# Kernel tuning notes

Measured on AMD Instinct MI355X. Metric: run time of the kernel, lower is better.

## Reference

```python
import jax, jax.numpy as jnp
import numpy as np

T = 1.0  # temperature (default in original forward)


def setup_inputs() -> dict:
    key = jax.random.key(0)
    k1, k2 = jax.random.split(key)
    N, M, D = 65536, 512, 256
    z = jax.random.normal(k1, (N, D), dtype=jnp.float32)
    e = jax.random.normal(k2, (M, D), dtype=jnp.float32)
    log_sigma = jnp.zeros((1,), dtype=jnp.float32)  # init_log_sigma = 0.0
    return {"z": z, "e": e, "log_sigma": log_sigma}


def reference(z, e, log_sigma):
    N, z_dim = z.shape
    M = e.shape[0]
    # pad N up to a multiple of M (zeros), then view as [B, M, z_dim]
    N_pad = ((N + M - 1) // M) * M
    z = jnp.pad(z, ((0, N_pad - N), (0, 0)))
    zb = z.reshape(-1, M, z_dim)  # [B, M, D]
    # squared euclidean distance via GEMM form: ||z||^2 + ||e||^2 - 2 z.e -> [B, M, M]
    dist = (
        jnp.sum(zb * zb, axis=-1)[:, :, None]
        + jnp.sum(e * e, axis=-1)[None, None, :]
        - 2.0 * jnp.einsum("bmd,kd->bmk", zb, e)
    )
    alpha = -1.0 / (2.0 * jnp.exp(log_sigma[0]) ** 2)
    # logsumexp over the z-block dim (axis=1), mean over codebook dim (axis=1 after reduce)
    loss = -jnp.mean(T * jax.nn.logsumexp(alpha * dist / T, axis=1), axis=1)  # [B]
    loss = loss + 0.5 * z_dim * (2.0 * log_sigma[0] - 1.0) + jnp.log(jnp.float32(M))
    return jnp.mean(loss)
```

## Files before the change

kernel.cpp:

```cpp
#include <hip/hip_runtime.h>
#include <stdint.h>
#include <math.h>

typedef __attribute__((ext_vector_type(8))) short short8;
typedef __attribute__((ext_vector_type(16))) float f32x16;

#define DEVI static __device__ __forceinline__

constexpr int D = 256;

constexpr size_t WS_EIMG  = 0;
constexpr size_t WS_ETERM = 262144;
constexpr size_t WS_WMAX  = 264192;
constexpr size_t WS_WSUM  = WS_WMAX + 1048576;
constexpr size_t WS_PART  = WS_WSUM + 1048576;

DEVI unsigned int f2bf(float f) {
  unsigned int u = __float_as_uint(f);
  return (u + 0x7fffu + ((u >> 16) & 1u)) >> 16;
}
DEVI float shflx(float v, int m) { return __shfl_xor(v, m, 64); }

__global__ void prep_e(const float* __restrict__ e, const float* __restrict__ lsp,
                       char* __restrict__ eimg, float* __restrict__ eterm) {
  const int et = blockIdx.x, t = threadIdx.x;
  const int c = t >> 3, o = t & 7;
  const int gc = et * 32 + c;
  const float a = __expf(-2.0f * lsp[0]);
  const float* s = e + (size_t)gc * D + o * 32;
  float sq = 0.0f;
  unsigned int w[16];
#pragma unroll
  for (int i = 0; i < 8; ++i) {
    float4 x = *(const float4*)(s + i * 4);
    sq += x.x * x.x + x.y * x.y + x.z * x.z + x.w * x.w;
    w[2 * i]     = f2bf(a * x.x) | (f2bf(a * x.y) << 16);
    w[2 * i + 1] = f2bf(a * x.z) | (f2bf(a * x.w) << 16);
  }
  sq += shflx(sq, 1); sq += shflx(sq, 2); sq += shflx(sq, 4);
  char* base = eimg + (size_t)et * 16384;
#pragma unroll
  for (int g = 0; g < 4; ++g) {
    int k2 = o * 4 + g;
    int phys = (c * 512 + k2 * 16) ^ ((c & 7) << 4);
    uint4 pk; pk.x = w[4 * g]; pk.y = w[4 * g + 1];
    pk.z = w[4 * g + 2]; pk.w = w[4 * g + 3];
    *(uint4*)(base + phys) = pk;
  }
  if (o == 0) eterm[gc] = -0.5f * a * sq;
}

__global__ __launch_bounds__(256, 2)
void lse_main(const float* __restrict__ z, const char* __restrict__ eimg,
              const float* __restrict__ lsp, float* __restrict__ wmax,
              float* __restrict__ wsum) {
  __shared__ char  ebuf[2][16384];
  __shared__ float zterm[128];
  __shared__ float pmaxb[2][4][32];
  __shared__ float psumb[2][4][32];

  const int tid = threadIdx.x;
  const int wid = tid >> 6, lane = tid & 63;
  const int l31 = lane & 31;
  const int hi  = lane >> 5;
  const int bx = blockIdx.x;
  const float a = __expf(-2.0f * lsp[0]);

  uint4 er[4];
#pragma unroll
  for (int i = 0; i < 4; ++i)
    er[i] = *(const uint4*)(eimg + i * 4096 + tid * 16);

  short8 A[16];
  const float* zs = z + ((size_t)bx * 128 + wid * 32 + l31) * D + hi * 8;
  float sq = 0.0f;
#pragma unroll
  for (int g = 0; g < 8; ++g) {
#pragma unroll
    for (int s2 = 0; s2 < 2; ++s2) {
      const int s = g * 2 + s2;
      float4 x0 = *(const float4*)(zs + s * 16);
      float4 x1 = *(const float4*)(zs + s * 16 + 4);
      sq += x0.x * x0.x + x0.y * x0.y + x0.z * x0.z + x0.w * x0.w +
            x1.x * x1.x + x1.y * x1.y + x1.z * x1.z + x1.w * x1.w;
      uint4 pk;
      pk.x = f2bf(x0.x) | (f2bf(x0.y) << 16);
      pk.y = f2bf(x0.z) | (f2bf(x0.w) << 16);
      pk.z = f2bf(x1.x) | (f2bf(x1.y) << 16);
      pk.w = f2bf(x1.z) | (f2bf(x1.w) << 16);
      A[s] = __builtin_bit_cast(short8, pk);
    }
    asm volatile("" ::: "memory");
  }
  sq += shflx(sq, 32);
  if (hi == 0) zterm[wid * 32 + l31] = -0.5f * a * sq;

#pragma unroll
  for (int i = 0; i < 4; ++i)
    *(uint4*)(&ebuf[0][0] + i * 4096 + tid * 16) = er[i];
  __syncthreads();

  float zt[16];
#pragma unroll
  for (int r = 0; r < 16; ++r)
    zt[r] = zterm[wid * 32 + (r & 3) + 8 * (r >> 2) + 4 * hi];

  const int cbase = l31 * 512;
  const int key = (l31 & 7) << 4;

  for (int p = 0; p < 16; ++p) {
    const int cur = p & 1;
    if (p < 15) {
#pragma unroll
      for (int i = 0; i < 4; ++i)
        er[i] = *(const uint4*)(eimg + (size_t)(p + 1) * 16384 + i * 4096 + tid * 16);
    }

    f32x16 acc;
#pragma unroll
    for (int i = 0; i < 16; ++i) acc[i] = 0.0f;
    const char* bp = &ebuf[cur][0];
#pragma unroll
    for (int s = 0; s < 16; ++s) {
      short8 B = *(const short8*)(bp + cbase + (((2 * s + hi) * 16) ^ key));
      acc = __builtin_amdgcn_mfma_f32_32x32x16_bf16(A[s], B, acc, 0, 0, 0);
    }

    float mx = -1e30f;
#pragma unroll
    for (int r = 0; r < 16; ++r) {
      acc[r] += zt[r];
      mx = fmaxf(mx, acc[r]);
    }
    mx = fmaxf(mx, shflx(mx, 32));
    float sme = 0.0f;
#pragma unroll
    for (int r = 0; r < 16; ++r) sme += __expf(acc[r] - mx);
    sme += shflx(sme, 32);
    if (hi == 0) {
      pmaxb[cur][wid][l31] = mx;
      psumb[cur][wid][l31] = sme;
    }
    if (p < 15) {
#pragma unroll
      for (int i = 0; i < 4; ++i)
        *(uint4*)(&ebuf[cur ^ 1][0] + i * 4096 + tid * 16) = er[i];
    }
    __syncthreads();

    if (tid < 32) {
      float m0 = pmaxb[cur][0][tid], m1 = pmaxb[cur][1][tid];
      float m2 = pmaxb[cur][2][tid], m3 = pmaxb[cur][3][tid];
      float nm = fmaxf(fmaxf(m0, m1), fmaxf(m2, m3));
      float s = psumb[cur][0][tid] * __expf(m0 - nm) +
                psumb[cur][1][tid] * __expf(m1 - nm) +
                psumb[cur][2][tid] * __expf(m2 - nm) +
                psumb[cur][3][tid] * __expf(m3 - nm);
      wmax[(size_t)bx * 512 + p * 32 + tid] = nm;
      wsum[(size_t)bx * 512 + p * 32 + tid] = s;
    }
  }
}

__global__ void merge_b(const float* __restrict__ wmax, const float* __restrict__ wsum,
                        const float* __restrict__ eterm, float* __restrict__ partial) {
  __shared__ float sh[512];
  const int b = blockIdx.x, t = threadIdx.x;
  float m[4];
  float nm = -1e30f;
#pragma unroll
  for (int i = 0; i < 4; ++i) {
    m[i] = wmax[(size_t)(4 * b + i) * 512 + t];
    nm = fmaxf(nm, m[i]);
  }
  float s = 0.0f;
#pragma unroll
  for (int i = 0; i < 4; ++i)
    s += wsum[(size_t)(4 * b + i) * 512 + t] * __expf(m[i] - nm);
  sh[t] = nm + logf(s) + eterm[t];
  __syncthreads();
  for (int st = 256; st > 0; st >>= 1) {
    if (t < st) sh[t] += sh[t + st];
    __syncthreads();
  }
  if (t == 0) partial[b] = sh[0];
}

__global__ void final_k(const float* __restrict__ partial,
                        const float* __restrict__ lsp, float* __restrict__ out) {
  __shared__ float sh[128];
  const int t = threadIdx.x;
  sh[t] = partial[t];
  __syncthreads();
  for (int st = 64; st > 0; st >>= 1) {
    if (t < st) sh[t] += sh[t + st];
    __syncthreads();
  }
  if (t == 0) {
    float ls = lsp[0];
    out[0] = -sh[0] / 65536.0f + 128.0f * (2.0f * ls - 1.0f) + logf(512.0f);
  }
}

extern "C" void kernel_launch(void* const* d_in, const int* in_sizes, int n_in,
                              void* d_out, int out_size, void* d_ws, size_t ws_size,
                              hipStream_t stream) {
  const float* z   = (const float*)d_in[0];
  const float* e   = (const float*)d_in[1];
  const float* lsp = (const float*)d_in[2];
  float* out = (float*)d_out;
  char* ws = (char*)d_ws;
  char*  eimg    = ws + WS_EIMG;
  float* eterm   = (float*)(ws + WS_ETERM);
  float* wmax    = (float*)(ws + WS_WMAX);
  float* wsum    = (float*)(ws + WS_WSUM);
  float* partial = (float*)(ws + WS_PART);

  prep_e<<<dim3(16), dim3(256), 0, stream>>>(e, lsp, eimg, eterm);
  lse_main<<<dim3(512), dim3(256), 0, stream>>>(z, eimg, lsp, wmax, wsum);
  merge_b<<<dim3(128), dim3(512), 0, stream>>>(wmax, wsum, eterm, partial);
  final_k<<<dim3(1), dim3(128), 0, stream>>>(partial, lsp, out);
}
```

Baseline: 45.49 us.

## Read codebook B-fragments directly from global memory, drop LDS staging and per-tile barriers

The prep kernel now writes the bf16 codebook in MFMA fragment order so each lane can load its B operand straight from global (L2-resident) memory. The main kernel no longer stages codebook tiles through double-buffered LDS and no longer synchronises after every 32-column tile. It processes two tiles per iteration with two independent MFMA accumulators and does one cross-wave merge at the end. This removes LDS traffic and 16 barriers per block, at the cost of more global/L2 load latency inside the MFMA loop and higher register pressure.

```diff
diff --git a/kernel.cpp b/kernel.cpp
--- a/kernel.cpp
+++ b/kernel.cpp
@@ -40,11 +40,11 @@
   sq += shflx(sq, 1); sq += shflx(sq, 2); sq += shflx(sq, 4);
   char* base = eimg + (size_t)et * 16384;
 #pragma unroll
-  for (int g = 0; g < 4; ++g) {
-    int k2 = o * 4 + g;
-    int phys = (c * 512 + k2 * 16) ^ ((c & 7) << 4);
-    uint4 pk; pk.x = w[4 * g]; pk.y = w[4 * g + 1];
-    pk.z = w[4 * g + 2]; pk.w = w[4 * g + 3];
+  for (int i = 0; i < 4; ++i) {
+    int g = o * 4 + i;
+    int phys = (g >> 1) * 1024 + (g & 1) * 512 + c * 16;
+    uint4 pk; pk.x = w[4 * i]; pk.y = w[4 * i + 1];
+    pk.z = w[4 * i + 2]; pk.w = w[4 * i + 3];
     *(uint4*)(base + phys) = pk;
   }
   if (o == 0) eterm[gc] = -0.5f * a * sq;
@@ -54,10 +54,8 @@
 void lse_main(const float* __restrict__ z, const char* __restrict__ eimg,
               const float* __restrict__ lsp, float* __restrict__ wmax,
               float* __restrict__ wsum) {
-  __shared__ char  ebuf[2][16384];
-  __shared__ float zterm[128];
-  __shared__ float pmaxb[2][4][32];
-  __shared__ float psumb[2][4][32];
+  __shared__ float sh_m[4][512];
+  __shared__ float sh_s[4][512];
 
   const int tid = threadIdx.x;
   const int wid = tid >> 6, lane = tid & 63;
@@ -65,11 +63,6 @@
   const int hi  = lane >> 5;
   const int bx = blockIdx.x;
   const float a = __expf(-2.0f * lsp[0]);
-
-  uint4 er[4];
-#pragma unroll
-  for (int i = 0; i < 4; ++i)
-    er[i] = *(const uint4*)(eimg + i * 4096 + tid * 16);
 
   short8 A[16];
   const float* zs = z + ((size_t)bx * 128 + wid * 32 + l31) * D + hi * 8;
@@ -93,72 +86,61 @@
     asm volatile("" ::: "memory");
   }
   sq += shflx(sq, 32);
-  if (hi == 0) zterm[wid * 32 + l31] = -0.5f * a * sq;
-
-#pragma unroll
-  for (int i = 0; i < 4; ++i)
-    *(uint4*)(&ebuf[0][0] + i * 4096 + tid * 16) = er[i];
+  const float term = -0.5f * a * sq;
+
+  float zt[16];
+#pragma unroll
+  for (int r = 0; r < 16; ++r)
+    zt[r] = __shfl(term, (r & 3) + 8 * (r >> 2) + 4 * hi, 64);
+
+  for (int p = 0; p < 8; ++p) {
+    const char* t0 = eimg + (size_t)(2 * p) * 16384 + lane * 16;
+    const char* t1 = t0 + 16384;
+
+    f32x16 acc0, acc1;
+#pragma unroll
+    for (int i = 0; i < 16; ++i) { acc0[i] = 0.0f; acc1[i] = 0.0f; }
+#pragma unroll
+    for (int s = 0; s < 16; ++s) {
+      short8 B0 = *(const short8*)(t0 + s * 1024);
+      short8 B1 = *(const short8*)(t1 + s * 1024);
+      acc0 = __builtin_amdgcn_mfma_f32_32x32x16_bf16(A[s], B0, acc0, 0, 0, 0);
+      acc1 = __builtin_amdgcn_mfma_f32_32x32x16_bf16(A[s], B1, acc1, 0, 0, 0);
+    }
+
+    float mx0 = -1e30f, mx1 = -1e30f;
+#pragma unroll
+    for (int r = 0; r < 16; ++r) {
+      acc0[r] += zt[r]; acc1[r] += zt[r];
+      mx0 = fmaxf(mx0, acc0[r]); mx1 = fmaxf(mx1, acc1[r]);
+    }
+    mx0 = fmaxf(mx0, shflx(mx0, 32));
+    mx1 = fmaxf(mx1, shflx(mx1, 32));
+    float sm0 = 0.0f, sm1 = 0.0f;
+#pragma unroll
+    for (int r = 0; r < 16; ++r) {
+      sm0 += __expf(acc0[r] - mx0);
+      sm1 += __expf(acc1[r] - mx1);
+    }
+    sm0 += shflx(sm0, 32);
+    sm1 += shflx(sm1, 32);
+    if (hi == 0) {
+      sh_m[wid][p * 64 + l31] = mx0;      sh_s[wid][p * 64 + l31] = sm0;
+      sh_m[wid][p * 64 + 32 + l31] = mx1; sh_s[wid][p * 64 + 32 + l31] = sm1;
+    }
+  }
+
   __syncthreads();
 
-  float zt[16];
-#pragma unroll
-  for (int r = 0; r < 16; ++r)
-    zt[r] = zterm[wid * 32 + (r & 3) + 8 * (r >> 2) + 4 * hi];
-
-  const int cbase = l31 * 512;
-  const int key = (l31 & 7) << 4;
-
-  for (int p = 0; p < 16; ++p) {
-    const int cur = p & 1;
-    if (p < 15) {
-#pragma unroll
-      for (int i = 0; i < 4; ++i)
-        er[i] = *(const uint4*)(eimg + (size_t)(p + 1) * 16384 + i * 4096 + tid * 16);
-    }
-
-    f32x16 acc;
-#pragma unroll
-    for (int i = 0; i < 16; ++i) acc[i] = 0.0f;
-    const char* bp = &ebuf[cur][0];
-#pragma unroll
-    for (int s = 0; s < 16; ++s) {
-      short8 B = *(const short8*)(bp + cbase + (((2 * s + hi) * 16) ^ key));
-      acc = __builtin_amdgcn_mfma_f32_32x32x16_bf16(A[s], B, acc, 0, 0, 0);
-    }
-
-    float mx = -1e30f;
-#pragma unroll
-    for (int r = 0; r < 16; ++r) {
-      acc[r] += zt[r];
-      mx = fmaxf(mx, acc[r]);
-    }
-    mx = fmaxf(mx, shflx(mx, 32));
-    float sme = 0.0f;
-#pragma unroll
-    for (int r = 0; r < 16; ++r) sme += __expf(acc[r] - mx);
-    sme += shflx(sme, 32);
-    if (hi == 0) {
-      pmaxb[cur][wid][l31] = mx;
-      psumb[cur][wid][l31] = sme;
-    }
-    if (p < 15) {
-#pragma unroll
-      for (int i = 0; i < 4; ++i)
-        *(uint4*)(&ebuf[cur ^ 1][0] + i * 4096 + tid * 16) = er[i];
-    }
-    __syncthreads();
-
-    if (tid < 32) {
-      float m0 = pmaxb[cur][0][tid], m1 = pmaxb[cur][1][tid];
-      float m2 = pmaxb[cur][2][tid], m3 = pmaxb[cur][3][tid];
-      float nm = fmaxf(fmaxf(m0, m1), fmaxf(m2, m3));
-      float s = psumb[cur][0][tid] * __expf(m0 - nm) +
-                psumb[cur][1][tid] * __expf(m1 - nm) +
-                psumb[cur][2][tid] * __expf(m2 - nm) +
-                psumb[cur][3][tid] * __expf(m3 - nm);
-      wmax[(size_t)bx * 512 + p * 32 + tid] = nm;
-      wsum[(size_t)bx * 512 + p * 32 + tid] = s;
-    }
+#pragma unroll
+  for (int h = 0; h < 2; ++h) {
+    const int c = h * 256 + tid;
+    float m0 = sh_m[0][c], m1 = sh_m[1][c], m2 = sh_m[2][c], m3 = sh_m[3][c];
+    float nm = fmaxf(fmaxf(m0, m1), fmaxf(m2, m3));
+    float s = sh_s[0][c] * __expf(m0 - nm) + sh_s[1][c] * __expf(m1 - nm) +
+              sh_s[2][c] * __expf(m2 - nm) + sh_s[3][c] * __expf(m3 - nm);
+    wmax[(size_t)bx * 512 + c] = nm;
+    wsum[(size_t)bx * 512 + c] = s;
   }
 }
 
```

After: 58.25 us. 28.0% more time.
